# Optimization experiments

Hardware: AMD Instinct MI355X
Metric: run time of the kernel (lower is better)

Reference implementation:

```python
import jax, jax.numpy as jnp
import numpy as np

SIZE = 512
K = 100000.0
EPS = 1e-05


def setup_inputs() -> dict:
    key = jax.random.key(0)
    contour = jax.random.uniform(key, (128, 2), dtype=jnp.float32)
    return {"contour": contour}


def reference(contour):
    size, k, eps = SIZE, K, EPS
    # mesh: (size^2, 1, 2), normalized pixel coordinates (ij indexing like torch.meshgrid)
    coords = jnp.arange(size, dtype=jnp.float32)
    mesh = jnp.stack(jnp.meshgrid(coords, coords, indexing="ij"), axis=-1)
    mesh = mesh.reshape(-1, 1, 2) / size

    diff = contour[None, :, :] - mesh              # (P, N, 2), P = size^2
    roll_diff = jnp.roll(diff, -1, axis=1)          # next contour point
    # roll by 1 along a size-2 axis == swap (x, y)
    prod = diff * roll_diff[:, :, ::-1]             # (P, N, 2)
    sign = jnp.tanh(k * (prod[:, :, 1] - prod[:, :, 0]))  # cross-product sign

    norm_diff = jnp.linalg.norm(diff, axis=2)
    norm_roll = jnp.linalg.norm(roll_diff, axis=2)
    scalar_product = jnp.sum(diff * roll_diff, axis=2)
    cos_ang = jnp.clip(scalar_product / (norm_diff * norm_roll), -1.0 + eps, 1.0 - eps)
    angles = jnp.arccos(cos_ang)                    # (P, N)

    sum_angles = jnp.clip(jnp.sum(sign * angles, axis=1) / (2.0 * jnp.pi), 0.0, 1.0)
    return sum_angles.reshape(1, 1, size, size)
```

## Files before the change

### kernel.cpp

```cpp
#include <hip/hip_runtime.h>
#include <math.h>

#define SIZE 512
#define NPTS 128

__global__ __launch_bounds__(256) void contour_mask_kernel(
    const float* __restrict__ contour, float* __restrict__ out)
{
    __shared__ float2 c[NPTS];

    const int tid = threadIdx.x;
    if (tid < NPTS) {
        c[tid] = ((const float2*)contour)[tid];
    }
    __syncthreads();

    const int p = blockIdx.x * 256 + tid;
    const int i = p >> 9;
    const int j = p & (SIZE - 1);

    const float mx = (float)i * (1.0f / SIZE);
    const float my = (float)j * (1.0f / SIZE);

    const float K    = 100000.0f;
    const float PI_F = 3.14159265358979f;
    const float HPI  = 1.57079632679490f;
    const float ANG_LO = 4.4721397e-3f;
    const float ANG_HI = 3.1371205f;
    const float CTHR = 6e-5f;

    float ax = c[0].x - mx;
    float ay = c[0].y - my;

    float acc = 0.0f;

    #pragma unroll 8
    for (int n = 0; n < NPTS; ++n) {
        const int n1 = (n + 1) & (NPTS - 1);
        const float2 cn = c[n1];
        const float bx = cn.x - mx;
        const float by = cn.y - my;

        const float cr = fmaf(ay, bx, -ax * by);
        const float dt = fmaf(ax, bx,  ay * by);

        const float acr = fabsf(cr), adt = fabsf(dt);
        const float mn  = fminf(acr, adt);
        const float mxv = fmaxf(acr, adt);
        const float t   = mn * __builtin_amdgcn_rcpf(mxv);
        const float s2  = t * t;

        float q = fmaf(-0.01172120f, s2, 0.05265332f);
        q = fmaf(q, s2, -0.11643287f);
        q = fmaf(q, s2,  0.19354346f);
        q = fmaf(q, s2, -0.33262347f);
        q = fmaf(q, s2,  0.99997726f);
        float a = t * q;

        a = (acr > adt) ? (HPI - a) : a;
        a = (dt < 0.0f) ? (PI_F - a) : a;
        a = __builtin_amdgcn_fmed3f(a, ANG_LO, ANG_HI);

        if (__any(acr < CTHR)) {
            const float e  = __expf(2.0f * K * cr);
            const float sg = fmaf(-2.0f, __builtin_amdgcn_rcpf(e + 1.0f), 1.0f);
            acc = fmaf(sg, a, acc);
        } else {
            acc += __builtin_copysignf(a, cr);
        }

        ax = bx; ay = by;
    }

    float r = acc * (1.0f / (2.0f * PI_F));
    out[p] = __builtin_amdgcn_fmed3f(r, 0.0f, 1.0f);
}

extern "C" void kernel_launch(void* const* d_in, const int* in_sizes, int n_in,
                              void* d_out, int out_size, void* d_ws, size_t ws_size,
                              hipStream_t stream) {
    const float* contour = (const float*)d_in[0];
    float* out = (float*)d_out;

    const int total = SIZE * SIZE;
    const int block = 256;
    const int grid  = total / block;

    contour_mask_kernel<<<grid, block, 0, stream>>>(contour, out);
}
```

Measured before the change: 76.11 us.

## Replace per-edge arccos sum with crossing-number winding plus near-edge correction

Computes the winding number with an integer crossing test for each edge (signed upward/downward crossings) in place of evaluating an atan polynomial on every edge. The full angle-and-tanh path runs only for groups of 8 edges where some lane has a near-zero cross product, and adds a correction for the clamp and tanh deviations. This removes most transcendental and polynomial work from the hot loop. The cost is redundant recomputation in flagged groups, plus a small risk of mismatch where the clamped angle sum differs from the exact winding.

```diff
diff --git a/kernel.cpp b/kernel.cpp
--- a/kernel.cpp
+++ b/kernel.cpp
@@ -7,12 +7,11 @@
 __global__ __launch_bounds__(256) void contour_mask_kernel(
     const float* __restrict__ contour, float* __restrict__ out)
 {
-    __shared__ float2 c[NPTS];
+    __shared__ float2 c[NPTS + 1];
 
     const int tid = threadIdx.x;
-    if (tid < NPTS) {
-        c[tid] = ((const float2*)contour)[tid];
-    }
+    if (tid < NPTS)  c[tid]  = ((const float2*)contour)[tid];
+    if (tid == NPTS) c[NPTS] = ((const float2*)contour)[0];
     __syncthreads();
 
     const int p = blockIdx.x * 256 + tid;
@@ -25,6 +24,7 @@
     const float K    = 100000.0f;
     const float PI_F = 3.14159265358979f;
     const float HPI  = 1.57079632679490f;
+    const float INV2PI = 0.15915494309190f;
     const float ANG_LO = 4.4721397e-3f;
     const float ANG_HI = 3.1371205f;
     const float CTHR = 6e-5f;
@@ -32,47 +32,64 @@
     float ax = c[0].x - mx;
     float ay = c[0].y - my;
 
-    float acc = 0.0f;
+    float w    = 0.0f;
+    float corr = 0.0f;
 
-    #pragma unroll 8
-    for (int n = 0; n < NPTS; ++n) {
-        const int n1 = (n + 1) & (NPTS - 1);
-        const float2 cn = c[n1];
-        const float bx = cn.x - mx;
-        const float by = cn.y - my;
+    #pragma unroll 1
+    for (int g = 0; g < NPTS / 8; ++g) {
+        const float gax = ax, gay = ay;
+        float bmin = 1e30f;
 
-        const float cr = fmaf(ay, bx, -ax * by);
-        const float dt = fmaf(ax, bx,  ay * by);
-
-        const float acr = fabsf(cr), adt = fabsf(dt);
-        const float mn  = fminf(acr, adt);
-        const float mxv = fmaxf(acr, adt);
-        const float t   = mn * __builtin_amdgcn_rcpf(mxv);
-        const float s2  = t * t;
-
-        float q = fmaf(-0.01172120f, s2, 0.05265332f);
-        q = fmaf(q, s2, -0.11643287f);
-        q = fmaf(q, s2,  0.19354346f);
-        q = fmaf(q, s2, -0.33262347f);
-        q = fmaf(q, s2,  0.99997726f);
-        float a = t * q;
-
-        a = (acr > adt) ? (HPI - a) : a;
-        a = (dt < 0.0f) ? (PI_F - a) : a;
-        a = __builtin_amdgcn_fmed3f(a, ANG_LO, ANG_HI);
-
-        if (__any(acr < CTHR)) {
-            const float e  = __expf(2.0f * K * cr);
-            const float sg = fmaf(-2.0f, __builtin_amdgcn_rcpf(e + 1.0f), 1.0f);
-            acc = fmaf(sg, a, acc);
-        } else {
-            acc += __builtin_copysignf(a, cr);
+        #pragma unroll
+        for (int k = 0; k < 8; ++k) {
+            const float2 cn = c[g * 8 + k + 1];
+            const float bx = cn.x - mx;
+            const float by = cn.y - my;
+            const float cr = fmaf(ay, bx, -ax * by);
+            const bool inc = (ay >  0.0f) & (by <= 0.0f) & (cr > 0.0f);
+            const bool dec = (ay <= 0.0f) & (by >  0.0f) & (cr < 0.0f);
+            w += inc ? 1.0f : 0.0f;
+            w -= dec ? 1.0f : 0.0f;
+            bmin = fminf(bmin, fabsf(cr));
+            ax = bx; ay = by;
         }
 
-        ax = bx; ay = by;
+        if (__any(bmin < CTHR)) {
+            float fax = gax, fay = gay;
+            #pragma unroll
+            for (int k = 0; k < 8; ++k) {
+                const float2 cn = c[g * 8 + k + 1];
+                const float bx = cn.x - mx;
+                const float by = cn.y - my;
+                const float cr = fmaf(fay, bx, -fax * by);
+                const float dt = fmaf(fax, bx,  fay * by);
+
+                const float acr = fabsf(cr), adt = fabsf(dt);
+                const float mn  = fminf(acr, adt);
+                const float mxv = fmaxf(acr, adt);
+                const float t   = mn * __builtin_amdgcn_rcpf(mxv);
+                const float s2  = t * t;
+                float q = fmaf(-0.01172120f, s2, 0.05265332f);
+                q = fmaf(q, s2, -0.11643287f);
+                q = fmaf(q, s2,  0.19354346f);
+                q = fmaf(q, s2, -0.33262347f);
+                q = fmaf(q, s2,  0.99997726f);
+                float an = t * q;
+                an = (acr > adt) ? (HPI  - an) : an;
+                an = (dt < 0.0f) ? (PI_F - an) : an;
+                const float anc = __builtin_amdgcn_fmed3f(an, ANG_LO, ANG_HI);
+
+                const float e  = __expf(2.0f * K * cr);
+                const float th = fmaf(-2.0f, __builtin_amdgcn_rcpf(e + 1.0f), 1.0f);
+
+                corr += fmaf(th, anc, -__builtin_copysignf(an, cr));
+
+                fax = bx; fay = by;
+            }
+        }
     }
 
-    float r = acc * (1.0f / (2.0f * PI_F));
+    const float r = fmaf(corr, INV2PI, w);
     out[p] = __builtin_amdgcn_fmed3f(r, 0.0f, 1.0f);
 }
 
```

New measurement: 73.49 us. 1.04x faster.
